# Performance work log

Hardware: AMD Instinct MI355X
Metric: run time of the kernel (lower is better)

Reference implementation:

```python
import jax, jax.numpy as jnp
import numpy as np

N_NODES = 50000
N_EDGES = 800000
IN_DIM = 128
HIDDEN = 128


def setup_inputs() -> dict:
    key = jax.random.key(0)
    ks = jax.random.split(key, 6)
    x = jax.random.normal(ks[0], (N_NODES, IN_DIM), dtype=jnp.float32)
    edge_index = jax.random.randint(ks[1], (2, N_EDGES), 0, N_NODES, dtype=jnp.int32)
    W1 = jax.random.normal(ks[2], (IN_DIM, HIDDEN), dtype=jnp.float32) * 0.05
    b1 = jnp.zeros((HIDDEN,), dtype=jnp.float32)
    W2 = jax.random.normal(ks[3], (HIDDEN, HIDDEN), dtype=jnp.float32) * 0.05
    b2 = jnp.zeros((HIDDEN,), dtype=jnp.float32)
    return {"x": x, "edge_index": edge_index, "W1": W1, "b1": b1, "W2": W2, "b2": b2}


def _gcn_conv(x, W, b, src, dst, norm, n):
    # PyG GCNConv: linear transform, then normalized sum-aggregate, then bias.
    h = x @ W                                  # [N, H]
    msg = h[src] * norm[:, None]               # gather + scale  [E+N, H]
    out = jax.ops.segment_sum(msg, dst, num_segments=n)
    return out + b


def reference(x, edge_index, W1, b1, W2, b2):
    n = x.shape[0]
    # add self-loops (GCNConv default add_self_loops=True)
    loops = jnp.arange(n, dtype=edge_index.dtype)
    src = jnp.concatenate([edge_index[0], loops])
    dst = jnp.concatenate([edge_index[1], loops])
    # symmetric normalization: deg over destination nodes (edge_weight = 1)
    deg = jax.ops.segment_sum(jnp.ones(src.shape, dtype=x.dtype), dst, num_segments=n)
    dinv = jax.lax.rsqrt(deg)                  # deg >= 1 because of self-loops
    norm = dinv[src] * dinv[dst]               # [E+N]
    h = jax.nn.relu(_gcn_conv(x, W1, b1, src, dst, norm, n))
    return _gcn_conv(h, W2, b2, src, dst, norm, n)
```

## Files before the change

kernel.cpp:

```cpp
#include <hip/hip_runtime.h>

#define N_NODES 50000
#define N_EDGES 800000
#define DIM 128
#define CHUNK 4096
#define GRID 196
#define SEG_CAP 6144
#define GEMM_BLOCKS 391
#define GA 316
#define GB (GEMM_BLOCKS - GA)

typedef __attribute__((ext_vector_type(8))) short bf16x8;
typedef __attribute__((ext_vector_type(4))) float f32x4;


__device__ inline unsigned rne_bf16(float f) {
    unsigned u = __float_as_uint(f);
    return (u + 0x7FFFu + ((u >> 16) & 1u)) >> 16;
}
__device__ inline unsigned pk_bf16(float a, float b) {
    return rne_bf16(a) | (rne_bf16(b) << 16);
}
__device__ inline float bf_lo(unsigned u) { return __uint_as_float(u << 16); }
__device__ inline float bf_hi(unsigned u) { return __uint_as_float(u & 0xFFFF0000u); }


__device__ void fragw_build(const float* __restrict__ W, uint4* __restrict__ fh,
                            uint4* __restrict__ fl, int slot) {
    const int lane = slot & 63, tile = slot >> 6;
    const int c = tile >> 2, q = tile & 3;
    const int k0 = q * 32 + ((lane >> 4) << 3);
    const int col = c * 16 + (lane & 15);
    unsigned h[8], l[8];
#pragma unroll
    for (int j = 0; j < 8; ++j) {
        float w = W[(size_t)(k0 + j) * DIM + col];
        unsigned hb = rne_bf16(w);
        h[j] = hb;
        l[j] = rne_bf16(w - __uint_as_float(hb << 16));
    }
    uint4 uh, ul;
    uh.x = h[0] | (h[1] << 16); uh.y = h[2] | (h[3] << 16);
    uh.z = h[4] | (h[5] << 16); uh.w = h[6] | (h[7] << 16);
    ul.x = l[0] | (l[1] << 16); ul.y = l[2] | (l[3] << 16);
    ul.z = l[4] | (l[5] << 16); ul.w = l[6] | (l[7] << 16);
    fh[slot] = uh;
    fl[slot] = ul;
}


__global__ __launch_bounds__(256) void chunk_hist_fragw(const int* __restrict__ dst,
                                                        int* __restrict__ chist,
                                                        const float* __restrict__ W1,
                                                        const float* __restrict__ W2,
                                                        uint4* f1h, uint4* f1l,
                                                        uint4* f2h, uint4* f2l) {
    const int bid = blockIdx.x;
    if (bid < GRID) {
        __shared__ int hist[256];
        const int t = threadIdx.x;
        const int eb = bid * CHUNK;
        const int cnt = min(CHUNK, N_EDGES - eb);
        hist[t] = 0;
        __syncthreads();
        for (int i = t; i < cnt; i += 256)
            atomicAdd(&hist[dst[eb + i] >> 8], 1);
        __syncthreads();
        chist[bid * 256 + t] = hist[t];
    } else {
        const int b2 = bid - GRID;
        const int slot = (b2 & 7) * 256 + threadIdx.x;
        if (b2 < 8) fragw_build(W1, f1h, f1l, slot);
        else        fragw_build(W2, f2h, f2l, slot);
    }
}


__device__ void gemm_body(const float* __restrict__ X,
                          const uint4* __restrict__ fWh,
                          const uint4* __restrict__ fWl,
                          uint2* __restrict__ O, int gb, char* smem) {
    const int t = threadIdx.x;

    {
        uint4* s4 = (uint4*)smem;
        for (int i = t; i < 2048; i += 256) {
            s4[i] = fWh[i];
            s4[2048 + i] = fWl[i];
        }
    }
    __syncthreads();

    const int w = t >> 6, lane = t & 63;
    const int lrow = lane & 15, lgrp = lane >> 4;
    const int rbase = gb * 128;

    bf16x8 Ah[2][4], Al[2][4];
#pragma unroll
    for (int m = 0; m < 2; ++m) {
        const int r = rbase + w * 32 + m * 16 + lrow;
        const bool ok = (r < N_NODES);
        const float4* xp = (const float4*)(X + (size_t)r * DIM + lgrp * 8);
#pragma unroll
        for (int q = 0; q < 4; ++q) {
            float4 a0 = ok ? xp[q * 8]     : make_float4(0.f, 0.f, 0.f, 0.f);
            float4 a1 = ok ? xp[q * 8 + 1] : make_float4(0.f, 0.f, 0.f, 0.f);
            float f[8] = {a0.x, a0.y, a0.z, a0.w, a1.x, a1.y, a1.z, a1.w};
            bf16x8 hi, lo;
#pragma unroll
            for (int j = 0; j < 8; ++j) {
                unsigned hb = rne_bf16(f[j]);
                hi[j] = (short)hb;
                lo[j] = (short)rne_bf16(f[j] - __uint_as_float(hb << 16));
            }
            Ah[m][q] = hi;
            Al[m][q] = lo;
        }
    }

    f32x4 acc[2][8];
#pragma unroll
    for (int m = 0; m < 2; ++m)
#pragma unroll
        for (int c = 0; c < 8; ++c)
            acc[m][c] = (f32x4){0.f, 0.f, 0.f, 0.f};

    const bf16x8* Bh = (const bf16x8*)smem;
    const bf16x8* Bl = (const bf16x8*)(smem + 32768);
#pragma unroll
    for (int c = 0; c < 8; ++c) {
#pragma unroll
        for (int q = 0; q < 4; ++q) {
            bf16x8 bh = Bh[(c * 4 + q) * 64 + lane];
            bf16x8 bl = Bl[(c * 4 + q) * 64 + lane];
#pragma unroll
            for (int m = 0; m < 2; ++m) {
                acc[m][c] = __builtin_amdgcn_mfma_f32_16x16x32_bf16(Ah[m][q], bh, acc[m][c], 0, 0, 0);
                acc[m][c] = __builtin_amdgcn_mfma_f32_16x16x32_bf16(Al[m][q], bh, acc[m][c], 0, 0, 0);
                acc[m][c] = __builtin_amdgcn_mfma_f32_16x16x32_bf16(Ah[m][q], bl, acc[m][c], 0, 0, 0);
            }
        }
    }

    __syncthreads();
    float* Lf = (float*)smem;
#pragma unroll
    for (int m = 0; m < 2; ++m)
#pragma unroll
        for (int c = 0; c < 8; ++c)
#pragma unroll
            for (int rg = 0; rg < 4; ++rg)
                Lf[(w * 32 + m * 16 + lgrp * 4 + rg) * DIM + c * 16 + lrow] = acc[m][c][rg];
    __syncthreads();

    const float4* Lf4 = (const float4*)smem;
    for (int idx = t; idx < 4096; idx += 256) {
        const int row = idx >> 5, s = idx & 31;
        const int gr = rbase + row;
        if (gr < N_NODES) {
            float4 v = Lf4[idx];
            uint2 o;
            o.x = pk_bf16(v.x, v.y);
            o.y = pk_bf16(v.z, v.w);
            O[(size_t)gr * 32 + s] = o;
        }
    }
}


__device__ void sort_scatter_body(const int* __restrict__ src,
                                  const int* __restrict__ dst,
                                  const int* __restrict__ chist,
                                  unsigned* __restrict__ sorted,
                                  int* __restrict__ bbase_g,
                                  int bid, char* smem) {
    int* hist  = (int*)smem;
    int* sc    = hist + 256;
    int* lbase = sc + 256;
    int* lcur  = lbase + 256;
    int* gbase = lcur + 256;
    unsigned* sl = (unsigned*)(smem + 5 * 1024);

    const int t = threadIdx.x;
    const int eb = bid * CHUNK;
    const int cnt = min(CHUNK, N_EDGES - eb);

    int sum = 0, myoff = 0;
    for (int c = 0; c < GRID; ++c) {
        int v = chist[c * 256 + t];
        if (c == bid) myoff = sum;
        sum += v;
    }
    hist[t] = chist[bid * 256 + t];
    sc[t] = sum;
    __syncthreads();
    for (int off = 1; off < 256; off <<= 1) {
        int u = (t >= off) ? sc[t - off] : 0;
        __syncthreads();
        sc[t] += u;
        __syncthreads();
    }
    gbase[t] = (sc[t] - sum) + myoff;
    if (bid == 0) bbase_g[t] = sc[t] - sum;
    __syncthreads();

    sc[t] = hist[t];
    __syncthreads();
    for (int off = 1; off < 256; off <<= 1) {
        int u = (t >= off) ? sc[t - off] : 0;
        __syncthreads();
        sc[t] += u;
        __syncthreads();
    }
    int ex = sc[t] - hist[t];
    lbase[t] = ex;
    lcur[t] = ex;
    __syncthreads();

    for (int i = t; i < cnt; i += 256) {
        int s = src[eb + i], d = dst[eb + i];
        int b = d >> 8;
        int p = atomicAdd(&lcur[b], 1);
        sl[p] = ((unsigned)b << 24) | ((unsigned)(d & 255) << 16) | (unsigned)s;
    }
    __syncthreads();
    for (int i = t; i < cnt; i += 256) {
        unsigned rec = sl[i];
        int b = rec >> 24;
        sorted[gbase[b] + (i - lbase[b])] = rec;
    }
}


__device__ void csr_build_body(const unsigned* __restrict__ sorted,
                               const int* __restrict__ bbase,
                               int* __restrict__ rowptr,
                               float* __restrict__ dinv,
                               int* __restrict__ csr,
                               int k, char* smem) {
    int* hist = (int*)smem;
    int* sc   = hist + 256;
    int* lcur = sc + 256;
    int* seg  = (int*)(smem + 3 * 1024);

    const int t = threadIdx.x;
    const int base = bbase[k];
    const int cntk = ((k == 255) ? N_EDGES : bbase[k + 1]) - base;
    if (k == 0 && t == 0) rowptr[N_NODES] = N_EDGES;

    hist[t] = 0;
    __syncthreads();
    for (int i = t; i < cntk; i += 256)
        atomicAdd(&hist[(sorted[base + i] >> 16) & 255], 1);
    __syncthreads();

    const int node = (k << 8) + t;
    const int dv = hist[t];
    if (node < N_NODES) dinv[node] = rsqrtf((float)dv + 1.0f);

    sc[t] = dv;
    __syncthreads();
    for (int off = 1; off < 256; off <<= 1) {
        int u = (t >= off) ? sc[t - off] : 0;
        __syncthreads();
        sc[t] += u;
        __syncthreads();
    }
    int ex = sc[t] - dv;
    if (node < N_NODES) rowptr[node] = base + ex;
    lcur[t] = ex;
    __syncthreads();

    if (cntk <= SEG_CAP) {
        for (int i = t; i < cntk; i += 256) {
            unsigned rec = sorted[base + i];
            int p = atomicAdd(&lcur[(rec >> 16) & 255], 1);
            seg[p] = (int)(rec & 0xFFFFu);
        }
        __syncthreads();
        for (int i = t; i < cntk; i += 256)
            csr[base + i] = seg[i];
    } else {
        for (int i = t; i < cntk; i += 256) {
            unsigned rec = sorted[base + i];
            int p = atomicAdd(&lcur[(rec >> 16) & 255], 1);
            csr[base + p] = (int)(rec & 0xFFFFu);
        }
    }
}


__global__ __launch_bounds__(256, 2) void sort_gemm(const int* __restrict__ src,
                                                    const int* __restrict__ dst,
                                                    const int* __restrict__ chist,
                                                    unsigned* __restrict__ sorted,
                                                    int* __restrict__ bbase_g,
                                                    const float* __restrict__ X,
                                                    const uint4* __restrict__ fWh,
                                                    const uint4* __restrict__ fWl,
                                                    uint2* __restrict__ O) {
    __shared__ __align__(16) char smem[65536];
    if (blockIdx.x < GRID)
        sort_scatter_body(src, dst, chist, sorted, bbase_g, blockIdx.x, smem);
    else
        gemm_body(X, fWh, fWl, O, blockIdx.x - GRID, smem);
}

__global__ __launch_bounds__(256, 2) void csr_gemm(const unsigned* __restrict__ sorted,
                                                   const int* __restrict__ bbase,
                                                   int* __restrict__ rowptr,
                                                   float* __restrict__ dinv,
                                                   int* __restrict__ csr,
                                                   const float* __restrict__ X,
                                                   const uint4* __restrict__ fWh,
                                                   const uint4* __restrict__ fWl,
                                                   uint2* __restrict__ O) {
    __shared__ __align__(16) char smem[65536];
    if (blockIdx.x < GRID)
        csr_build_body(sorted, bbase, rowptr, dinv, csr, blockIdx.x, smem);
    else
        gemm_body(X, fWh, fWl, O, blockIdx.x - GRID + GA, smem);
}


#define ACC8_D(v, d) do { \
        a0 = fmaf((d), bf_lo((v).x), a0); a1 = fmaf((d), bf_hi((v).x), a1); \
        a2 = fmaf((d), bf_lo((v).y), a2); a3 = fmaf((d), bf_hi((v).y), a3); \
        a4 = fmaf((d), bf_lo((v).z), a4); a5 = fmaf((d), bf_hi((v).z), a5); \
        a6 = fmaf((d), bf_lo((v).w), a6); a7 = fmaf((d), bf_hi((v).w), a7); } while (0)

#define ACC8_P(v) do { \
        a0 += bf_lo((v).x); a1 += bf_hi((v).x); \
        a2 += bf_lo((v).y); a3 += bf_hi((v).y); \
        a4 += bf_lo((v).z); a5 += bf_hi((v).z); \
        a6 += bf_lo((v).w); a7 += bf_hi((v).w); } while (0)


__global__ __launch_bounds__(256) void aggregate_h1(const uint2* __restrict__ H2,
                                                    const int* __restrict__ rowptr,
                                                    const int* __restrict__ csr,
                                                    const float* __restrict__ dinv,
                                                    const float4* __restrict__ b4,
                                                    uint4* __restrict__ h1h4,
                                                    uint4* __restrict__ h1l4) {
    const int node = blockIdx.x * 4 + (threadIdx.x >> 6);
    if (node >= N_NODES) return;
    const int lane = threadIdx.x & 63;
    const int q = lane >> 4, l16 = lane & 15;
    const uint4* H4 = (const uint4*)H2;

    const float dn = dinv[node];
    float a0 = 0.f, a1 = 0.f, a2 = 0.f, a3 = 0.f,
          a4 = 0.f, a5 = 0.f, a6 = 0.f, a7 = 0.f;
    if (q == 0) {
        uint4 v = H4[(size_t)node * 16 + l16];
        ACC8_D(v, dn);
    }

    int j = rowptr[node];
    const int end = rowptr[node + 1];
    for (; j + 8 <= end; j += 8) {
        int s0 = csr[j + q], s1 = csr[j + 4 + q];
        uint4 v0 = H4[(size_t)s0 * 16 + l16]; float d0 = dinv[s0];
        uint4 v1 = H4[(size_t)s1 * 16 + l16]; float d1 = dinv[s1];
        ACC8_D(v0, d0); ACC8_D(v1, d1);
    }
    if (j + 4 <= end) {
        int s = csr[j + q];
        uint4 v = H4[(size_t)s * 16 + l16]; float d = dinv[s];
        ACC8_D(v, d);
        j += 4;
    }
    if (q < end - j) {
        int s = csr[j + q];
        uint4 v = H4[(size_t)s * 16 + l16]; float d = dinv[s];
        ACC8_D(v, d);
    }

    a0 += __shfl_xor(a0, 16, 64); a1 += __shfl_xor(a1, 16, 64);
    a2 += __shfl_xor(a2, 16, 64); a3 += __shfl_xor(a3, 16, 64);
    a4 += __shfl_xor(a4, 16, 64); a5 += __shfl_xor(a5, 16, 64);
    a6 += __shfl_xor(a6, 16, 64); a7 += __shfl_xor(a7, 16, 64);
    a0 += __shfl_xor(a0, 32, 64); a1 += __shfl_xor(a1, 32, 64);
    a2 += __shfl_xor(a2, 32, 64); a3 += __shfl_xor(a3, 32, 64);
    a4 += __shfl_xor(a4, 32, 64); a5 += __shfl_xor(a5, 32, 64);
    a6 += __shfl_xor(a6, 32, 64); a7 += __shfl_xor(a7, 32, 64);

    if (lane < 16) {
        float4 bbA = b4[l16 * 2], bbB = b4[l16 * 2 + 1];
        float o0 = fmaxf(a0 * dn + bbA.x, 0.f), o1 = fmaxf(a1 * dn + bbA.y, 0.f);
        float o2 = fmaxf(a2 * dn + bbA.z, 0.f), o3 = fmaxf(a3 * dn + bbA.w, 0.f);
        float o4 = fmaxf(a4 * dn + bbB.x, 0.f), o5 = fmaxf(a5 * dn + bbB.y, 0.f);
        float o6 = fmaxf(a6 * dn + bbB.z, 0.f), o7 = fmaxf(a7 * dn + bbB.w, 0.f);
        o0 *= dn; o1 *= dn; o2 *= dn; o3 *= dn;
        o4 *= dn; o5 *= dn; o6 *= dn; o7 *= dn;
        unsigned h0 = rne_bf16(o0), h1 = rne_bf16(o1), h2 = rne_bf16(o2), h3 = rne_bf16(o3);
        unsigned h4 = rne_bf16(o4), h5 = rne_bf16(o5), h6 = rne_bf16(o6), h7 = rne_bf16(o7);
        uint4 hv;
        hv.x = h0 | (h1 << 16); hv.y = h2 | (h3 << 16);
        hv.z = h4 | (h5 << 16); hv.w = h6 | (h7 << 16);
        uint4 lv;
        lv.x = rne_bf16(o0 - __uint_as_float(h0 << 16)) |
               (rne_bf16(o1 - __uint_as_float(h1 << 16)) << 16);
        lv.y = rne_bf16(o2 - __uint_as_float(h2 << 16)) |
               (rne_bf16(o3 - __uint_as_float(h3 << 16)) << 16);
        lv.z = rne_bf16(o4 - __uint_as_float(h4 << 16)) |
               (rne_bf16(o5 - __uint_as_float(h5 << 16)) << 16);
        lv.w = rne_bf16(o6 - __uint_as_float(h6 << 16)) |
               (rne_bf16(o7 - __uint_as_float(h7 << 16)) << 16);
        h1h4[(size_t)node * 16 + l16] = hv;
        h1l4[(size_t)node * 16 + l16] = lv;
    }
}


__global__ __launch_bounds__(256) void aggregate_out(const uint2* __restrict__ H2,
                                                     const int* __restrict__ rowptr,
                                                     const int* __restrict__ csr,
                                                     const float* __restrict__ dinv,
                                                     const float4* __restrict__ b4,
                                                     float4* __restrict__ out) {
    const int node = blockIdx.x * 4 + (threadIdx.x >> 6);
    if (node >= N_NODES) return;
    const int lane = threadIdx.x & 63;
    const int q = lane >> 4, l16 = lane & 15;
    const uint4* H4 = (const uint4*)H2;

    float a0 = 0.f, a1 = 0.f, a2 = 0.f, a3 = 0.f,
          a4 = 0.f, a5 = 0.f, a6 = 0.f, a7 = 0.f;
    if (q == 0) {
        uint4 v = H4[(size_t)node * 16 + l16];
        ACC8_P(v);
    }

    int j = rowptr[node];
    const int end = rowptr[node + 1];
    for (; j + 8 <= end; j += 8) {
        int s0 = csr[j + q], s1 = csr[j + 4 + q];
        uint4 v0 = H4[(size_t)s0 * 16 + l16];
        uint4 v1 = H4[(size_t)s1 * 16 + l16];
        ACC8_P(v0); ACC8_P(v1);
    }
    if (j + 4 <= end) {
        int s = csr[j + q];
        uint4 v = H4[(size_t)s * 16 + l16];
        ACC8_P(v);
        j += 4;
    }
    if (q < end - j) {
        int s = csr[j + q];
        uint4 v = H4[(size_t)s * 16 + l16];
        ACC8_P(v);
    }

    a0 += __shfl_xor(a0, 16, 64); a1 += __shfl_xor(a1, 16, 64);
    a2 += __shfl_xor(a2, 16, 64); a3 += __shfl_xor(a3, 16, 64);
    a4 += __shfl_xor(a4, 16, 64); a5 += __shfl_xor(a5, 16, 64);
    a6 += __shfl_xor(a6, 16, 64); a7 += __shfl_xor(a7, 16, 64);
    a0 += __shfl_xor(a0, 32, 64); a1 += __shfl_xor(a1, 32, 64);
    a2 += __shfl_xor(a2, 32, 64); a3 += __shfl_xor(a3, 32, 64);
    a4 += __shfl_xor(a4, 32, 64); a5 += __shfl_xor(a5, 32, 64);
    a6 += __shfl_xor(a6, 32, 64); a7 += __shfl_xor(a7, 32, 64);

    if (lane < 16) {
        const float dn = dinv[node];
        float4 bbA = b4[l16 * 2], bbB = b4[l16 * 2 + 1];
        float4 oA, oB;
        oA.x = a0 * dn + bbA.x; oA.y = a1 * dn + bbA.y;
        oA.z = a2 * dn + bbA.z; oA.w = a3 * dn + bbA.w;
        oB.x = a4 * dn + bbB.x; oB.y = a5 * dn + bbB.y;
        oB.z = a6 * dn + bbB.z; oB.w = a7 * dn + bbB.w;
        out[(size_t)node * 32 + l16 * 2]     = oA;
        out[(size_t)node * 32 + l16 * 2 + 1] = oB;
    }
}


__global__ __launch_bounds__(256, 2) void gemm_xw2(const uint2* __restrict__ h1h,
                                                   const uint2* __restrict__ h1l,
                                                   const uint4* __restrict__ fWh,
                                                   const uint4* __restrict__ fWl,
                                                   uint2* __restrict__ O) {
    __shared__ __align__(16) char smem[65536];
    const int t = threadIdx.x;

    {
        uint4* s4 = (uint4*)smem;
        for (int i = t; i < 2048; i += 256) {
            s4[i] = fWh[i];
            s4[2048 + i] = fWl[i];
        }
    }
    __syncthreads();

    const int w = t >> 6, lane = t & 63;
    const int lrow = lane & 15, lgrp = lane >> 4;
    const int rbase = blockIdx.x * 128;

    bf16x8 Ah[2][4], Al[2][4];
    const bf16x8 zz = (bf16x8){0,0,0,0,0,0,0,0};
#pragma unroll
    for (int m = 0; m < 2; ++m) {
        const int r = rbase + w * 32 + m * 16 + lrow;
        const bool ok = (r < N_NODES);
        const uint2* ph = h1h + (size_t)r * 32 + lgrp * 2;
        const uint2* pl = h1l + (size_t)r * 32 + lgrp * 2;
#pragma unroll
        for (int q = 0; q < 4; ++q) {
            Ah[m][q] = ok ? *(const bf16x8*)(ph + q * 8) : zz;
            Al[m][q] = ok ? *(const bf16x8*)(pl + q * 8) : zz;
        }
    }

    f32x4 acc[2][8];
#pragma unroll
    for (int m = 0; m < 2; ++m)
#pragma unroll
        for (int c = 0; c < 8; ++c)
            acc[m][c] = (f32x4){0.f, 0.f, 0.f, 0.f};

    const bf16x8* Bh = (const bf16x8*)smem;
    const bf16x8* Bl = (const bf16x8*)(smem + 32768);
#pragma unroll
    for (int c = 0; c < 8; ++c) {
#pragma unroll
        for (int q = 0; q < 4; ++q) {
            bf16x8 bh = Bh[(c * 4 + q) * 64 + lane];
            bf16x8 bl = Bl[(c * 4 + q) * 64 + lane];
#pragma unroll
            for (int m = 0; m < 2; ++m) {
                acc[m][c] = __builtin_amdgcn_mfma_f32_16x16x32_bf16(Ah[m][q], bh, acc[m][c], 0, 0, 0);
                acc[m][c] = __builtin_amdgcn_mfma_f32_16x16x32_bf16(Al[m][q], bh, acc[m][c], 0, 0, 0);
                acc[m][c] = __builtin_amdgcn_mfma_f32_16x16x32_bf16(Ah[m][q], bl, acc[m][c], 0, 0, 0);
            }
        }
    }

    __syncthreads();
    float* Lf = (float*)smem;
#pragma unroll
    for (int m = 0; m < 2; ++m)
#pragma unroll
        for (int c = 0; c < 8; ++c)
#pragma unroll
            for (int rg = 0; rg < 4; ++rg)
                Lf[(w * 32 + m * 16 + lgrp * 4 + rg) * DIM + c * 16 + lrow] = acc[m][c][rg];
    __syncthreads();

    const float4* Lf4 = (const float4*)smem;
    for (int idx = t; idx < 4096; idx += 256) {
        const int row = idx >> 5, s = idx & 31;
        const int gr = rbase + row;
        if (gr < N_NODES) {
            float4 v = Lf4[idx];
            uint2 o;
            o.x = pk_bf16(v.x, v.y);
            o.y = pk_bf16(v.z, v.w);
            O[(size_t)gr * 32 + s] = o;
        }
    }
}


extern "C" void kernel_launch(void* const* d_in, const int* in_sizes, int n_in,
                              void* d_out, int out_size, void* d_ws, size_t ws_size,
                              hipStream_t stream) {
    const float* x  = (const float*)d_in[0];
    const int*   ei = (const int*)d_in[1];
    const float* W1 = (const float*)d_in[2];
    const float* b1 = (const float*)d_in[3];
    const float* W2 = (const float*)d_in[4];
    const float* b2 = (const float*)d_in[5];
    float* out = (float*)d_out;

    const int* src = ei;
    const int* dst = ei + N_EDGES;

    char* p = (char*)d_ws;
    int*      chist  = (int*)p;              p += GRID * 256 * 4;
    float*    dinv   = (float*)p;            p += ((N_NODES * 4 + 1023) & ~1023);
    int*      rowptr = (int*)p;              p += (((N_NODES + 1) * 4 + 1023) & ~1023);
    unsigned* sorted = (unsigned*)p;         p += ((N_EDGES * 4 + 1023) & ~1023);
    int*      csr    = (int*)p;              p += ((N_EDGES * 4 + 1023) & ~1023);
    int*      bbase  = (int*)p;              p += 1024;
    uint4*    f1h    = (uint4*)p;            p += 32768;
    uint4*    f1l    = (uint4*)p;            p += 32768;
    uint4*    f2h    = (uint4*)p;            p += 32768;
    uint4*    f2l    = (uint4*)p;            p += 32768;
    uint2*    hp     = (uint2*)p;            p += (size_t)N_NODES * DIM * 2;
    uint2*    h1h    = (uint2*)p;            p += (size_t)N_NODES * DIM * 2;
    uint2*    h1l    = (uint2*)p;            p += (size_t)N_NODES * DIM * 2;
    uint2*    hp2    = (uint2*)p;

    const int aggBlocks = (N_NODES + 3) / 4;

    chunk_hist_fragw<<<GRID + 16, 256, 0, stream>>>(dst, chist, W1, W2,
                                                    f1h, f1l, f2h, f2l);
    sort_gemm<<<GRID + GA, 256, 0, stream>>>(src, dst, chist, sorted, bbase,
                                             x, f1h, f1l, hp);
    csr_gemm<<<GRID + GB, 256, 0, stream>>>(sorted, bbase, rowptr, dinv, csr,
                                            x, f1h, f1l, hp);

    aggregate_h1<<<aggBlocks, 256, 0, stream>>>(hp, rowptr, csr, dinv,
                                                (const float4*)b1,
                                                (uint4*)h1h, (uint4*)h1l);

    gemm_xw2<<<GEMM_BLOCKS, 256, 0, stream>>>(h1h, h1l, f2h, f2l, hp2);

    aggregate_out<<<aggBlocks, 256, 0, stream>>>(hp2, rowptr, csr, dinv,
                                                 (const float4*)b2, (float4*)out);
}
```

Baseline: 203.5 us.

## Read GEMM weight fragments from global memory and halve LDS staging

The GEMM bodies no longer stage the W hi/lo fragments in LDS and instead load them directly from global memory, relying on cache hits. The output transpose buffer now handles one 16-row half at a time, which cuts shared memory from 64KB to 32KB per block so more blocks can be resident. All layer-1 GEMM blocks move into the sort kernel, and CSR construction becomes its own kernel with no GEMM work attached. The trade-off is more global/L2 traffic for B fragments, an extra barrier round, and a changed overlap between CSR building and the GEMM.

```diff
diff --git a/kernel.cpp b/kernel.cpp
--- a/kernel.cpp
+++ b/kernel.cpp
@@ -7,8 +7,7 @@
 #define GRID 196
 #define SEG_CAP 6144
 #define GEMM_BLOCKS 391
-#define GA 316
-#define GB (GEMM_BLOCKS - GA)
+#define GA 391
 
 typedef __attribute__((ext_vector_type(8))) short bf16x8;
 typedef __attribute__((ext_vector_type(4))) float f32x4;
@@ -81,16 +80,6 @@
                           const uint4* __restrict__ fWl,
                           uint2* __restrict__ O, int gb, char* smem) {
     const int t = threadIdx.x;
-
-    {
-        uint4* s4 = (uint4*)smem;
-        for (int i = t; i < 2048; i += 256) {
-            s4[i] = fWh[i];
-            s4[2048 + i] = fWl[i];
-        }
-    }
-    __syncthreads();
-
     const int w = t >> 6, lane = t & 63;
     const int lrow = lane & 15, lgrp = lane >> 4;
     const int rbase = gb * 128;
@@ -125,8 +114,8 @@
         for (int c = 0; c < 8; ++c)
             acc[m][c] = (f32x4){0.f, 0.f, 0.f, 0.f};
 
-    const bf16x8* Bh = (const bf16x8*)smem;
-    const bf16x8* Bl = (const bf16x8*)(smem + 32768);
+    const bf16x8* Bh = (const bf16x8*)fWh;
+    const bf16x8* Bl = (const bf16x8*)fWl;
 #pragma unroll
     for (int c = 0; c < 8; ++c) {
 #pragma unroll
@@ -142,27 +131,27 @@
         }
     }
 
-    __syncthreads();
     float* Lf = (float*)smem;
 #pragma unroll
-    for (int m = 0; m < 2; ++m)
+    for (int m = 0; m < 2; ++m) {
+        __syncthreads();
 #pragma unroll
         for (int c = 0; c < 8; ++c)
 #pragma unroll
             for (int rg = 0; rg < 4; ++rg)
-                Lf[(w * 32 + m * 16 + lgrp * 4 + rg) * DIM + c * 16 + lrow] = acc[m][c][rg];
-    __syncthreads();
-
-    const float4* Lf4 = (const float4*)smem;
-    for (int idx = t; idx < 4096; idx += 256) {
-        const int row = idx >> 5, s = idx & 31;
-        const int gr = rbase + row;
-        if (gr < N_NODES) {
-            float4 v = Lf4[idx];
-            uint2 o;
-            o.x = pk_bf16(v.x, v.y);
-            o.y = pk_bf16(v.z, v.w);
-            O[(size_t)gr * 32 + s] = o;
+                Lf[(w * 16 + lgrp * 4 + rg) * 128 + c * 16 + lrow] = acc[m][c][rg];
+        __syncthreads();
+        const float4* Lf4 = (const float4*)smem;
+        for (int idx = t; idx < 2048; idx += 256) {
+            const int rl = idx >> 5, s = idx & 31;
+            const int gr = rbase + (rl >> 4) * 32 + m * 16 + (rl & 15);
+            if (gr < N_NODES) {
+                float4 v = Lf4[idx];
+                uint2 o;
+                o.x = pk_bf16(v.x, v.y);
+                o.y = pk_bf16(v.z, v.w);
+                O[(size_t)gr * 32 + s] = o;
+            }
         }
     }
 }
@@ -232,17 +221,18 @@
 }
 
 
-__device__ void csr_build_body(const unsigned* __restrict__ sorted,
-                               const int* __restrict__ bbase,
-                               int* __restrict__ rowptr,
-                               float* __restrict__ dinv,
-                               int* __restrict__ csr,
-                               int k, char* smem) {
+__global__ __launch_bounds__(256) void csr_build(const unsigned* __restrict__ sorted,
+                                                 const int* __restrict__ bbase,
+                                                 int* __restrict__ rowptr,
+                                                 float* __restrict__ dinv,
+                                                 int* __restrict__ csr) {
+    __shared__ __align__(16) char smem[3 * 1024 + SEG_CAP * 4];
     int* hist = (int*)smem;
     int* sc   = hist + 256;
     int* lcur = sc + 256;
     int* seg  = (int*)(smem + 3 * 1024);
 
+    const int k = blockIdx.x;
     const int t = threadIdx.x;
     const int base = bbase[k];
     const int cntk = ((k == 255) ? N_EDGES : bbase[k + 1]) - base;
@@ -290,36 +280,20 @@
 }
 
 
-__global__ __launch_bounds__(256, 2) void sort_gemm(const int* __restrict__ src,
-                                                    const int* __restrict__ dst,
-                                                    const int* __restrict__ chist,
-                                                    unsigned* __restrict__ sorted,
-                                                    int* __restrict__ bbase_g,
-                                                    const float* __restrict__ X,
-                                                    const uint4* __restrict__ fWh,
-                                                    const uint4* __restrict__ fWl,
-                                                    uint2* __restrict__ O) {
-    __shared__ __align__(16) char smem[65536];
+__global__ __launch_bounds__(256) void sort_gemm(const int* __restrict__ src,
+                                                 const int* __restrict__ dst,
+                                                 const int* __restrict__ chist,
+                                                 unsigned* __restrict__ sorted,
+                                                 int* __restrict__ bbase_g,
+                                                 const float* __restrict__ X,
+                                                 const uint4* __restrict__ fWh,
+                                                 const uint4* __restrict__ fWl,
+                                                 uint2* __restrict__ O) {
+    __shared__ __align__(16) char smem[32768];
     if (blockIdx.x < GRID)
         sort_scatter_body(src, dst, chist, sorted, bbase_g, blockIdx.x, smem);
     else
         gemm_body(X, fWh, fWl, O, blockIdx.x - GRID, smem);
-}
-
-__global__ __launch_bounds__(256, 2) void csr_gemm(const unsigned* __restrict__ sorted,
-                                                   const int* __restrict__ bbase,
-                                                   int* __restrict__ rowptr,
-                                                   float* __restrict__ dinv,
-                                                   int* __restrict__ csr,
-                                                   const float* __restrict__ X,
-                                                   const uint4* __restrict__ fWh,
-                                                   const uint4* __restrict__ fWl,
-                                                   uint2* __restrict__ O) {
-    __shared__ __align__(16) char smem[65536];
-    if (blockIdx.x < GRID)
-        csr_build_body(sorted, bbase, rowptr, dinv, csr, blockIdx.x, smem);
-    else
-        gemm_body(X, fWh, fWl, O, blockIdx.x - GRID + GA, smem);
 }
 
 
@@ -476,23 +450,13 @@
 }
 
 
-__global__ __launch_bounds__(256, 2) void gemm_xw2(const uint2* __restrict__ h1h,
-                                                   const uint2* __restrict__ h1l,
-                                                   const uint4* __restrict__ fWh,
-                                                   const uint4* __restrict__ fWl,
-                                                   uint2* __restrict__ O) {
-    __shared__ __align__(16) char smem[65536];
+__global__ __launch_bounds__(256) void gemm_xw2(const uint2* __restrict__ h1h,
+                                                const uint2* __restrict__ h1l,
+                                                const uint4* __restrict__ fWh,
+                                                const uint4* __restrict__ fWl,
+                                                uint2* __restrict__ O) {
+    __shared__ __align__(16) char smem[32768];
     const int t = threadIdx.x;
-
-    {
-        uint4* s4 = (uint4*)smem;
-        for (int i = t; i < 2048; i += 256) {
-            s4[i] = fWh[i];
-            s4[2048 + i] = fWl[i];
-        }
-    }
-    __syncthreads();
-
     const int w = t >> 6, lane = t & 63;
     const int lrow = lane & 15, lgrp = lane >> 4;
     const int rbase = blockIdx.x * 128;
@@ -519,8 +483,8 @@
         for (int c = 0; c < 8; ++c)
             acc[m][c] = (f32x4){0.f, 0.f, 0.f, 0.f};
 
-    const bf16x8* Bh = (const bf16x8*)smem;
-    const bf16x8* Bl = (const bf16x8*)(smem + 32768);
+    const bf16x8* Bh = (const bf16x8*)fWh;
+    const bf16x8* Bl = (const bf16x8*)fWl;
 #pragma unroll
     for (int c = 0; c < 8; ++c) {
 #pragma unroll
@@ -536,27 +500,27 @@
         }
     }
 
-    __syncthreads();
     float* Lf = (float*)smem;
 #pragma unroll
-    for (int m = 0; m < 2; ++m)
+    for (int m = 0; m < 2; ++m) {
+        __syncthreads();
 #pragma unroll
         for (int c = 0; c < 8; ++c)
 #pragma unroll
             for (int rg = 0; rg < 4; ++rg)
-                Lf[(w * 32 + m * 16 + lgrp * 4 + rg) * DIM + c * 16 + lrow] = acc[m][c][rg];
-    __syncthreads();
-
-    const float4* Lf4 = (const float4*)smem;
-    for (int idx = t; idx < 4096; idx += 256) {
-        const int row = idx >> 5, s = idx & 31;
-        const int gr = rbase + row;
-        if (gr < N_NODES) {
-            float4 v = Lf4[idx];
-            uint2 o;
-            o.x = pk_bf16(v.x, v.y);
-            o.y = pk_bf16(v.z, v.w);
-            O[(size_t)gr * 32 + s] = o;
+                Lf[(w * 16 + lgrp * 4 + rg) * 128 + c * 16 + lrow] = acc[m][c][rg];
+        __syncthreads();
+        const float4* Lf4 = (const float4*)smem;
+        for (int idx = t; idx < 2048; idx += 256) {
+            const int rl = idx >> 5, s = idx & 31;
+            const int gr = rbase + (rl >> 4) * 32 + m * 16 + (rl & 15);
+            if (gr < N_NODES) {
+                float4 v = Lf4[idx];
+                uint2 o;
+                o.x = pk_bf16(v.x, v.y);
+                o.y = pk_bf16(v.z, v.w);
+                O[(size_t)gr * 32 + s] = o;
+            }
         }
     }
 }
@@ -598,8 +562,7 @@
                                                     f1h, f1l, f2h, f2l);
     sort_gemm<<<GRID + GA, 256, 0, stream>>>(src, dst, chist, sorted, bbase,
                                              x, f1h, f1l, hp);
-    csr_gemm<<<GRID + GB, 256, 0, stream>>>(sorted, bbase, rowptr, dinv, csr,
-                                            x, f1h, f1l, hp);
+    csr_build<<<GRID, 256, 0, stream>>>(sorted, bbase, rowptr, dinv, csr);
 
     aggregate_h1<<<aggBlocks, 256, 0, stream>>>(hp, rowptr, csr, dinv,
                                                 (const float4*)b1,
```

Result: no change. 206.8 us (+1.6%).
